# Optimization experiments

Measured on AMD Instinct MI355X. Metric: run time of the kernel, lower is better.

## Reference

```python
import jax, jax.numpy as jnp
import numpy as np

M1 = M2 = M3 = 12   # Fourier modes kept per dim
WID = 32            # channel width
NL = 4              # number of Fourier layers
HID = 128           # skip-block hidden
INF = 9             # coord_dim + param_dim


def _gelu(x):
    return jax.nn.gelu(x, approximate=False)  # torch F.gelu default is exact erf


def _spectral_conv3d(x, w1, w2, w3, w4):
    # x: [B, Cin, S, V, T]; weights: [Cin, Cout, M1, M2, M3, 2]
    B, Ci, S, Vd, T = x.shape
    x_ft = jnp.fft.rfftn(x, axes=(-3, -2, -1))  # [B,Ci,S,V,T//2+1] complex64

    def cmul(sub, w):
        wc = w[..., 0] + 1j * w[..., 1]
        return jnp.einsum('bixyz,ioxyz->boxyz', sub, wc)

    Co = w1.shape[1]
    out_ft = jnp.zeros((B, Co, S, Vd, T // 2 + 1), dtype=x_ft.dtype)
    out_ft = out_ft.at[:, :, :M1, :M2, :M3].set(cmul(x_ft[:, :, :M1, :M2, :M3], w1))
    out_ft = out_ft.at[:, :, -M1:, :M2, :M3].set(cmul(x_ft[:, :, -M1:, :M2, :M3], w2))
    out_ft = out_ft.at[:, :, :M1, -M2:, :M3].set(cmul(x_ft[:, :, :M1, -M2:, :M3], w3))
    out_ft = out_ft.at[:, :, -M1:, -M2:, :M3].set(cmul(x_ft[:, :, -M1:, -M2:, :M3], w4))
    return jnp.fft.irfftn(out_ft, s=(S, Vd, T), axes=(-3, -2, -1))


def setup_inputs() -> dict:
    key = jax.random.key(0)
    ks = jax.random.split(key, 24)
    B, S, Vd, T = 4, 64, 64, 64
    scale = 1.0 / (WID * WID)
    spec_shape = (NL, WID, WID, M1, M2, M3, 2)
    inp = {
        'coords': jax.random.uniform(ks[0], (B, S, Vd, T, 3), dtype=jnp.float32),
        'params': jax.random.normal(ks[1], (B, 6), dtype=jnp.float32),
        'lift_w': 0.3 * jax.random.normal(ks[2], (INF, WID), dtype=jnp.float32),
        'lift_b': jnp.zeros((WID,), jnp.float32),
        'spec_w1': scale * jax.random.uniform(ks[3], spec_shape, dtype=jnp.float32),
        'spec_w2': scale * jax.random.uniform(ks[4], spec_shape, dtype=jnp.float32),
        'spec_w3': scale * jax.random.uniform(ks[5], spec_shape, dtype=jnp.float32),
        'spec_w4': scale * jax.random.uniform(ks[6], spec_shape, dtype=jnp.float32),
        'conv_w': 0.15 * jax.random.normal(ks[7], (NL, WID, WID), dtype=jnp.float32),
        'conv_b': jnp.zeros((NL, WID), jnp.float32),
        's1w': 0.3 * jax.random.normal(ks[8], (NL, INF, HID), dtype=jnp.float32),
        's1b': jnp.zeros((NL, HID), jnp.float32),
        's2w': 0.09 * jax.random.normal(ks[9], (NL, HID, HID), dtype=jnp.float32),
        's2b': jnp.zeros((NL, HID), jnp.float32),
        's3w': 0.09 * jax.random.normal(ks[10], (NL, HID, WID), dtype=jnp.float32),
        's3b': jnp.zeros((NL, WID), jnp.float32),
        'p1w': 0.15 * jax.random.normal(ks[11], (WID, WID // 2), dtype=jnp.float32),
        'p1b': jnp.zeros((WID // 2,), jnp.float32),
        'p2w': 0.25 * jax.random.normal(ks[12], (WID // 2, 1), dtype=jnp.float32),
        'p2b': jnp.zeros((1,), jnp.float32),
    }
    return inp


def reference(coords, params, lift_w, lift_b, spec_w1, spec_w2, spec_w3, spec_w4,
              conv_w, conv_b, s1w, s1b, s2w, s2b, s3w, s3b, p1w, p1b, p2w, p2b):
    B, S, Vd, T, _ = coords.shape
    # coordinate lift: broadcast params over grid, concat -> [B,S,V,T,9]
    pexp = jnp.broadcast_to(params[:, None, None, None, :], (B, S, Vd, T, params.shape[-1]))
    z = jnp.concatenate([coords, pexp], axis=-1)
    x = z @ lift_w + lift_b                      # [B,S,V,T,W]
    x = jnp.transpose(x, (0, 4, 1, 2, 3))        # [B,W,S,V,T]
    for i in range(NL):
        x1 = _spectral_conv3d(x, spec_w1[i], spec_w2[i], spec_w3[i], spec_w4[i])
        x2 = jnp.einsum('bixyz,oi->boxyz', x, conv_w[i]) + conv_b[i][None, :, None, None, None]
        xf = _gelu(x1 + x2)
        skip = _gelu(z @ s1w[i] + s1b[i])
        skip = _gelu(skip @ s2w[i] + s2b[i])
        skip = skip @ s3w[i] + s3b[i]            # [B,S,V,T,W]
        x = xf + jnp.transpose(skip, (0, 4, 1, 2, 3))
    x = jnp.transpose(x, (0, 2, 3, 4, 1))        # [B,S,V,T,W]
    h = _gelu(x @ p1w + p1b)
    out = (h @ p2w + p2b)[..., 0]                # [B,S,V,T]
    return out
```

## Files before the change

### kernel.cpp

```cpp
#include <hip/hip_runtime.h>
#include <hip/hip_bf16.h>
#include <math.h>

#define NB   4
#define NC   32
#define SVT  262144
#define VT   4096
#define NLAY 4
#define TWOPI_64 0.09817477042468103f

typedef __attribute__((ext_vector_type(8))) short bf16x8;
typedef __attribute__((ext_vector_type(4))) float f32x4;
typedef __attribute__((ext_vector_type(4))) unsigned short us4;

__device__ __forceinline__ float gelu_f(float x){
    float x2 = x * x;
    float u  = x * __builtin_fmaf(-0.10294322f, x2, -2.30220795f);
    float e  = __builtin_amdgcn_exp2f(u);
    return x * __builtin_amdgcn_rcpf(1.0f + e);
}

__device__ __forceinline__ unsigned short f2bf(float f){
    union { __hip_bfloat16 h; unsigned short u; } cv;
    cv.h = __float2bfloat16(f);
    return cv.u;
}
__device__ __forceinline__ float bf2f(unsigned short u){
    return __uint_as_float(((unsigned int)u) << 16);
}

__global__ __launch_bounds__(256) void k_prep(
    const float* __restrict__ s1w, const float* __restrict__ s2w,
    const float* __restrict__ s3w,
    unsigned short* __restrict__ w1bf,
    unsigned short* __restrict__ w2bf,
    unsigned short* __restrict__ w3bf,
    unsigned short* __restrict__ tdft)
{
    int g = blockIdx.x * 256 + threadIdx.x;
    if (g < 65536){
        int l = g >> 14, r = g & 16383;
        int c = r >> 7, k = r & 127;
        w2bf[g] = f2bf(s2w[l*16384 + k*128 + c]);
        return;
    }
    int g3 = g - 65536;
    if (g3 < 16384){
        int l = g3 >> 12, r = g3 & 4095;
        int c2 = r >> 7, k = r & 127;
        w3bf[g3] = f2bf(s3w[l*4096 + k*32 + c2]);
        return;
    }
    int g1 = g3 - 16384;
    if (g1 < 4608){ w1bf[g1] = f2bf(s1w[g1]); return; }
    int g4 = g1 - 4608;
    if (g4 < 2048){
        int o = g4 >> 6, t = g4 & 63;
        float val = 0.f;
        if (o < 24){
            int kz = o >> 1;
            float ang = (float)((kz * t) & 63) * TWOPI_64;
            float sn, cs; sincosf(ang, &sn, &cs);
            val = (o & 1) ? -sn : cs;
        }
        unsigned short h = f2bf(val);
        tdft[g4]        = h;
        tdft[2048 + g4] = f2bf(val - bf2f(h));
    }
}

__global__ __launch_bounds__(256) void k_lift(
    const float* __restrict__ coords, const float* __restrict__ params,
    const float* __restrict__ lw, const float* __restrict__ lb,
    float* __restrict__ x)
{
    size_t g = (size_t)blockIdx.x * 256 + threadIdx.x;
    int b = (int)(g >> 18);
    size_t p = g & (size_t)(SVT - 1);
    float z[9];
    z[0] = coords[g*3+0]; z[1] = coords[g*3+1]; z[2] = coords[g*3+2];
    #pragma unroll
    for (int j = 0; j < 6; ++j) z[3+j] = params[b*6+j];
    #pragma unroll
    for (int c = 0; c < 32; ++c){
        float acc = lb[c];
        #pragma unroll
        for (int j = 0; j < 9; ++j) acc += z[j] * lw[j*32 + c];
        x[(size_t)(b*32 + c) * SVT + p] = acc;
    }
}

__global__ __launch_bounds__(256) void k_fwdTV(
    const float* __restrict__ x, const unsigned short* __restrict__ tdft,
    float2* __restrict__ X2)
{
    __shared__ __align__(16) unsigned short Ahi[64][72], Alo[64][72];
    __shared__ __align__(16) unsigned short Bhi[32][72], Blo[32][72];
    __shared__ float2 a2[12][66];
    __shared__ float2 wtab[64];
    int tid = threadIdx.x;
    int bc = blockIdx.x >> 6;
    int s  = blockIdx.x & 63;
    if (tid < 64){
        float sn, cs;
        sincosf((float)tid * TWOPI_64, &sn, &cs);
        wtab[tid] = make_float2(cs, sn);
    }
    for (int i = tid; i < 2048; i += 256){
        int o = i >> 6, t = i & 63;
        Bhi[o][t] = tdft[i];
        Blo[o][t] = tdft[2048 + i];
    }
    {
        int row = tid >> 2, c0 = (tid & 3) << 4;
        const float* src = x + (size_t)bc * SVT + (size_t)s * VT + row*64 + c0;
        #pragma unroll
        for (int q = 0; q < 4; ++q){
            float4 v4 = *(const float4*)&src[q*4];
            float vv[4] = {v4.x, v4.y, v4.z, v4.w};
            #pragma unroll
            for (int e = 0; e < 4; ++e){
                unsigned short h = f2bf(vv[e]);
                Ahi[row][c0 + q*4 + e] = h;
                Alo[row][c0 + q*4 + e] = f2bf(vv[e] - bf2f(h));
            }
        }
    }
    __syncthreads();
    int l = tid & 63, w = tid >> 6;
    int lr = l & 15, kg = l >> 4;
    int r0 = w << 4;
    f32x4 acc[2];
    acc[0] = (f32x4){0.f,0.f,0.f,0.f}; acc[1] = (f32x4){0.f,0.f,0.f,0.f};
    #pragma unroll
    for (int kc = 0; kc < 2; ++kc){
        int ko = kc*32 + kg*8;
        bf16x8 ah = *(const bf16x8*)&Ahi[r0 + lr][ko];
        bf16x8 al = *(const bf16x8*)&Alo[r0 + lr][ko];
        #pragma unroll
        for (int n = 0; n < 2; ++n){
            bf16x8 bh = *(const bf16x8*)&Bhi[n*16 + lr][ko];
            bf16x8 bl = *(const bf16x8*)&Blo[n*16 + lr][ko];
            acc[n] = __builtin_amdgcn_mfma_f32_16x16x32_bf16(ah, bh, acc[n], 0, 0, 0);
            acc[n] = __builtin_amdgcn_mfma_f32_16x16x32_bf16(ah, bl, acc[n], 0, 0, 0);
            acc[n] = __builtin_amdgcn_mfma_f32_16x16x32_bf16(al, bh, acc[n], 0, 0, 0);
        }
    }
    #pragma unroll
    for (int n = 0; n < 2; ++n){
        int o = n*16 + lr;
        if (o < 24){
            int kz = o >> 1;
            #pragma unroll
            for (int r = 0; r < 4; ++r){
                int v = r0 + kg*4 + r;
                if (o & 1) a2[kz][v].y = acc[n][r];
                else       a2[kz][v].x = acc[n][r];
            }
        }
    }
    __syncthreads();
    for (int task = tid; task < 288; task += 256){
        int kz = task % 12;
        int ky = task / 12;
        int kya = (ky < 12) ? ky : ky + 40;
        float re = 0.f, im = 0.f;
        for (int v = 0; v < 64; ++v){
            float2 wv = wtab[(kya * v) & 63];
            float2 a  = a2[kz][v];
            re += a.x * wv.x + a.y * wv.y;
            im += a.y * wv.x - a.x * wv.y;
        }
        X2[((size_t)(bc*12 + kz) * 24 + ky) * 64 + s] = make_float2(re, im);
    }
}

__global__ __launch_bounds__(256) void k_fwdS(
    const float2* __restrict__ X2, float2* __restrict__ X3)
{
    __shared__ float2 cin[32][65];
    __shared__ float2 wtab[64];
    int tid = threadIdx.x;
    if (tid < 64){
        float sn, cs; sincosf((float)tid * TWOPI_64, &sn, &cs);
        wtab[tid] = make_float2(cs, sn);
    }
    int rbase = blockIdx.x * 32;
    for (int i = tid; i < 2048; i += 256){
        int row = i >> 6, s = i & 63;
        cin[row][s] = X2[(size_t)(rbase + row) * 64 + s];
    }
    __syncthreads();
    int row = tid & 31;
    int r = rbase + row;
    int kxg = tid >> 5;
    int kxs[3];
    #pragma unroll
    for (int j = 0; j < 3; ++j){ int kxi = kxg*3 + j; kxs[j] = (kxi < 12) ? kxi : kxi + 40; }
    float re[3] = {0,0,0}, im[3] = {0,0,0};
    for (int s = 0; s < 64; ++s){
        float2 cv = cin[row][s];
        #pragma unroll
        for (int j = 0; j < 3; ++j){
            float2 wv = wtab[(kxs[j] * s) & 63];
            re[j] += cv.x * wv.x + cv.y * wv.y;
            im[j] += cv.y * wv.x - cv.x * wv.y;
        }
    }
    int bc = r / 288; int kz = (r / 24) % 12; int ky = r % 24;
    #pragma unroll
    for (int j = 0; j < 3; ++j){
        int kxi = kxg*3 + j;
        X3[(size_t)bc * 6912 + (size_t)kxi * 288 + ky * 12 + kz] = make_float2(re[j], im[j]);
    }
}

__global__ __launch_bounds__(256) void k_modemix(
    const float2* __restrict__ X3,
    const float* __restrict__ w1, const float* __restrict__ w2,
    const float* __restrict__ w3, const float* __restrict__ w4,
    int layer, float2* __restrict__ Y)
{
    __shared__ float2 wlds[32][64];
    int tid = threadIdx.x;
    int m   = tid & 63;
    int b   = tid >> 6;
    int corner = blockIdx.y >> 3;
    int o0     = (blockIdx.y & 7) * 4;
    int moff0  = blockIdx.x * 64;
    const float* wsrc = (corner==0 ? w1 : corner==1 ? w2 : corner==2 ? w3 : w4)
                        + (size_t)layer * 3538944;
    int moff = moff0 + m;
    int m1  = moff / 144;
    int rem = moff - m1 * 144;
    int kx  = m1 + ((corner == 1 || corner == 3) ? 12 : 0);
    int mode_g = kx * 288 + rem + ((corner >= 2) ? 144 : 0);

    float xr[32], xi[32];
    const float2* xp = X3 + (size_t)b * 32 * 6912 + mode_g;
    #pragma unroll
    for (int i = 0; i < 32; ++i){
        float2 a = xp[(size_t)i * 6912];
        xr[i] = a.x; xi[i] = a.y;
    }
    for (int oo = 0; oo < 4; ++oo){
        int o = o0 + oo;
        __syncthreads();
        for (int j = tid; j < 2048; j += 256){
            int i = j >> 6, mm = j & 63;
            wlds[i][mm] = *(const float2*)&wsrc[((size_t)(i*32 + o) * 1728 + moff0 + mm) * 2];
        }
        __syncthreads();
        float re = 0.f, im = 0.f;
        #pragma unroll
        for (int i = 0; i < 32; ++i){
            float2 wv = wlds[i][m];
            re += xr[i]*wv.x - xi[i]*wv.y;
            im += xr[i]*wv.y + xi[i]*wv.x;
        }
        Y[(size_t)(b*32 + o) * 6912 + mode_g] = make_float2(re, im);
    }
}

__global__ __launch_bounds__(256) void k_invS(
    const float2* __restrict__ Y, float2* __restrict__ Z1)
{
    __shared__ float2 yin[24][24];
    __shared__ float2 wtab[64];
    int tid = threadIdx.x;
    if (tid < 64){
        float sn, cs; sincosf((float)tid * TWOPI_64, &sn, &cs);
        wtab[tid] = make_float2(cs, sn);
    }
    int bo = blockIdx.x / 12;
    int kz = blockIdx.x % 12;
    for (int i = tid; i < 576; i += 256){
        int kx = i / 24, ky = i % 24;
        yin[kx][ky] = Y[(size_t)bo * 6912 + (size_t)kx * 288 + ky * 12 + kz];
    }
    __syncthreads();
    int s = tid & 63;
    int kyg = tid >> 6;
    float re[6] = {0,0,0,0,0,0}, im[6] = {0,0,0,0,0,0};
    for (int kxi = 0; kxi < 24; ++kxi){
        int kxa = (kxi < 12) ? kxi : kxi + 40;
        float2 wv = wtab[(kxa * s) & 63];
        #pragma unroll
        for (int j = 0; j < 6; ++j){
            float2 a = yin[kxi][kyg*6 + j];
            re[j] += a.x * wv.x - a.y * wv.y;
            im[j] += a.x * wv.y + a.y * wv.x;
        }
    }
    #pragma unroll
    for (int j = 0; j < 6; ++j){
        int ky = kyg*6 + j;
        Z1[((size_t)(bo*12 + kz) * 64 + s) * 24 + ky] = make_float2(re[j], im[j]);
    }
}

__global__ __launch_bounds__(256) void k_conv(
    float* x, const float* __restrict__ cw,
    const float* __restrict__ cb, int layer)
{
    __shared__ float wsh[32][32];
    __shared__ float bsh[32];
    int tid = threadIdx.x;
    if (tid < 32) bsh[tid] = cb[layer*32 + tid];
    for (int i = tid; i < 1024; i += 256) wsh[i >> 5][i & 31] = cw[layer*1024 + i];
    __syncthreads();
    size_t g = (size_t)blockIdx.x * 256 + tid;
    int b = (int)(g >> 18);
    size_t p = g & (size_t)(SVT - 1);
    float acc[32];
    #pragma unroll
    for (int o = 0; o < 32; ++o) acc[o] = bsh[o];
    for (int i = 0; i < 32; ++i){
        float xv = x[(size_t)(b*32 + i) * SVT + p];
        #pragma unroll
        for (int o = 0; o < 32; ++o) acc[o] += xv * wsh[o][i];
    }
    #pragma unroll
    for (int o = 0; o < 32; ++o) x[(size_t)(b*32 + o) * SVT + p] = acc[o];
}

__global__ __launch_bounds__(256) void k_invVT(
    const float2* __restrict__ Z1, float* xio)
{
    __shared__ float2 zin[12][24];
    __shared__ float2 c2[12][66];
    __shared__ float2 wtab[64];
    int tid = threadIdx.x;
    int bo = blockIdx.x >> 6;
    int s  = blockIdx.x & 63;
    if (tid < 64){
        float sn, cs; sincosf((float)tid * TWOPI_64, &sn, &cs);
        wtab[tid] = make_float2(cs, sn);
    }
    for (int i = tid; i < 288; i += 256){
        int kz = i / 24, ky = i % 24;
        zin[kz][ky] = Z1[((size_t)(bo*12 + kz) * 64 + s) * 24 + ky];
    }
    __syncthreads();
    #pragma unroll
    for (int j = 0; j < 3; ++j){
        int task = tid + j * 256;
        int v = task & 63, kz = task >> 6;
        float re = 0.f, im = 0.f;
        #pragma unroll
        for (int ky = 0; ky < 24; ++ky){
            int kya = (ky < 12) ? ky : ky + 40;
            float2 wv = wtab[(kya * v) & 63];
            float2 a = zin[kz][ky];
            re += a.x * wv.x - a.y * wv.y;
            im += a.x * wv.y + a.y * wv.x;
        }
        c2[kz][v] = make_float2(re, im);
    }
    __syncthreads();
    int v  = tid & 63;
    int tb = (tid >> 6) << 4;
    float sum[16];
    #pragma unroll
    for (int j = 0; j < 16; ++j) sum[j] = 0.f;
    float dc = c2[0][v].x;
    #pragma unroll
    for (int kz = 1; kz < 12; ++kz){
        float2 a = c2[kz][v];
        #pragma unroll
        for (int j = 0; j < 16; ++j){
            float2 wv = wtab[(kz * (tb + j)) & 63];
            sum[j] += a.x * wv.x - a.y * wv.y;
        }
    }
    const float norm = 1.0f / 262144.0f;
    size_t base = (size_t)bo * SVT + (size_t)s * VT + (size_t)v * 64 + tb;
    #pragma unroll
    for (int j = 0; j < 16; j += 4){
        float4 xv = *(const float4*)&xio[base + j];
        float4 r;
        r.x = gelu_f((dc + 2.f*sum[j+0]) * norm + xv.x);
        r.y = gelu_f((dc + 2.f*sum[j+1]) * norm + xv.y);
        r.z = gelu_f((dc + 2.f*sum[j+2]) * norm + xv.z);
        r.w = gelu_f((dc + 2.f*sum[j+3]) * norm + xv.w);
        *(float4*)&xio[base + j] = r;
    }
}

template<int LAST>
__global__ __launch_bounds__(256) void k_skip(
    const float* __restrict__ coords, const float* __restrict__ params,
    const unsigned short* __restrict__ w1bf, const float* __restrict__ s1b,
    const unsigned short* __restrict__ w2bf, const float* __restrict__ s2b,
    const unsigned short* __restrict__ w3bf, const float* __restrict__ s3b,
    int layer, float* __restrict__ xio,
    const float* __restrict__ p1w, const float* __restrict__ p1b,
    const float* __restrict__ p2w, const float* __restrict__ p2b,
    float* __restrict__ out)
{
    __shared__ __align__(16) unsigned short A1[64][136];
    __shared__ __align__(16) unsigned short zst[4][16][8];
    __shared__ __align__(16) unsigned short w1pk[128][8];
    __shared__ unsigned short w1s[9][128];
    __shared__ float pb[128];
    __shared__ float b2s[128];
    __shared__ float b3s[32];

    int tid = threadIdx.x;
    size_t g0 = (size_t)blockIdx.x * 64;
    int b = (int)(g0 >> 18);
    const unsigned short* w2g = w2bf + (size_t)layer * 16384;
    const unsigned short* w3g = w3bf + (size_t)layer * 4096;

    for (int i = tid; i < 1152; i += 256) w1s[i >> 7][i & 127] = w1bf[layer*1152 + i];
    if (tid < 128) b2s[tid] = s2b[layer*128 + tid];
    if (tid < 32)  b3s[tid] = s3b[layer*32  + tid];
    __syncthreads();
    if (tid < 128){
        float acc = s1b[layer*128 + tid];
        #pragma unroll
        for (int j = 0; j < 6; ++j) acc += params[b*6 + j] * bf2f(w1s[3 + j][tid]);
        pb[tid] = acc;
        bf16x8 pk;
        pk[0] = (short)w1s[0][tid]; pk[1] = (short)w1s[1][tid];
        pk[2] = (short)w1s[2][tid]; pk[3] = 0;
        pk[4] = pk[0]; pk[5] = pk[1]; pk[6] = pk[2]; pk[7] = 0;
        *(bf16x8*)&w1pk[tid][0] = pk;
    }
    __syncthreads();

    int l  = tid & 63;
    int w  = tid >> 6;
    int lr = l & 15;
    int kg = l >> 4;

    if (l < 16){
        size_t g = g0 + w*16 + l;
        float z0 = coords[g*3+0], z1 = coords[g*3+1], z2 = coords[g*3+2];
        unsigned short h0 = f2bf(z0), h1 = f2bf(z1), h2 = f2bf(z2);
        bf16x8 pk;
        pk[0] = (short)h0; pk[1] = (short)h1; pk[2] = (short)h2; pk[3] = 0;
        pk[4] = (short)f2bf(z0 - bf2f(h0));
        pk[5] = (short)f2bf(z1 - bf2f(h1));
        pk[6] = (short)f2bf(z2 - bf2f(h2));
        pk[7] = 0;
        *(bf16x8*)&zst[w][l][0] = pk;
    }
    bf16x8 bz;
    if (kg == 0) bz = *(const bf16x8*)&zst[w][lr][0];
    else         bz = (bf16x8){0,0,0,0,0,0,0,0};

    {
        f32x4 accB[8];
        #pragma unroll
        for (int m = 0; m < 8; ++m) accB[m] = (f32x4){0.f,0.f,0.f,0.f};
        #pragma unroll
        for (int m = 0; m < 8; ++m){
            bf16x8 af = *(const bf16x8*)&w1pk[m*16 + lr][0];
            accB[m] = __builtin_amdgcn_mfma_f32_16x16x32_bf16(af, bz, accB[m], 0, 0, 0);
        }
        #pragma unroll
        for (int m = 0; m < 8; ++m){
            int c0 = m*16 + kg*4;
            float4 bb = *(const float4*)&pb[c0];
            us4 pk4;
            pk4[0] = f2bf(gelu_f(accB[m][0] + bb.x));
            pk4[1] = f2bf(gelu_f(accB[m][1] + bb.y));
            pk4[2] = f2bf(gelu_f(accB[m][2] + bb.z));
            pk4[3] = f2bf(gelu_f(accB[m][3] + bb.w));
            *(us4*)&A1[w*16 + lr][c0] = pk4;
        }
    }
    __syncthreads();

    f32x4 accC[2][4];
    #pragma unroll
    for (int mi = 0; mi < 2; ++mi)
        #pragma unroll
        for (int pt = 0; pt < 4; ++pt) accC[mi][pt] = (f32x4){0.f,0.f,0.f,0.f};
    #pragma unroll
    for (int kc = 0; kc < 4; ++kc){
        int ko = kc*32 + kg*8;
        bf16x8 a0 = *(const bf16x8*)&w2g[((2*w    )*16 + lr)*128 + ko];
        bf16x8 a1 = *(const bf16x8*)&w2g[((2*w + 1)*16 + lr)*128 + ko];
        #pragma unroll
        for (int pt = 0; pt < 4; ++pt){
            bf16x8 bb = *(const bf16x8*)&A1[pt*16 + lr][ko];
            accC[0][pt] = __builtin_amdgcn_mfma_f32_16x16x32_bf16(a0, bb, accC[0][pt], 0, 0, 0);
            accC[1][pt] = __builtin_amdgcn_mfma_f32_16x16x32_bf16(a1, bb, accC[1][pt], 0, 0, 0);
        }
    }
    __syncthreads();
    #pragma unroll
    for (int mi = 0; mi < 2; ++mi)
        #pragma unroll
        for (int pt = 0; pt < 4; ++pt){
            int c0 = (2*w + mi)*16 + kg*4;
            float4 bb = *(const float4*)&b2s[c0];
            us4 pk4;
            pk4[0] = f2bf(gelu_f(accC[mi][pt][0] + bb.x));
            pk4[1] = f2bf(gelu_f(accC[mi][pt][1] + bb.y));
            pk4[2] = f2bf(gelu_f(accC[mi][pt][2] + bb.z));
            pk4[3] = f2bf(gelu_f(accC[mi][pt][3] + bb.w));
            *(us4*)&A1[pt*16 + lr][c0] = pk4;
        }
    __syncthreads();

    int nD  = w & 1;
    int pt0 = (w >> 1) * 2;
    f32x4 c3[2];
    c3[0] = (f32x4){0.f,0.f,0.f,0.f}; c3[1] = (f32x4){0.f,0.f,0.f,0.f};
    #pragma unroll
    for (int kc = 0; kc < 4; ++kc){
        int ko = kc*32 + kg*8;
        bf16x8 bw3 = *(const bf16x8*)&w3g[(nD*16 + lr)*128 + ko];
        bf16x8 aa0 = *(const bf16x8*)&A1[(pt0    )*16 + lr][ko];
        bf16x8 aa1 = *(const bf16x8*)&A1[(pt0 + 1)*16 + lr][ko];
        c3[0] = __builtin_amdgcn_mfma_f32_16x16x32_bf16(aa0, bw3, c3[0], 0, 0, 0);
        c3[1] = __builtin_amdgcn_mfma_f32_16x16x32_bf16(aa1, bw3, c3[1], 0, 0, 0);
    }
    __syncthreads();

    float* outsT = (float*)&A1[0][0];
    {
        int c2 = nD*16 + lr;
        float bv = b3s[c2];
        #pragma unroll
        for (int q = 0; q < 2; ++q){
            int p0 = (pt0 + q)*16 + kg*4;
            float4 v4;
            v4.x = c3[q][0] + bv; v4.y = c3[q][1] + bv;
            v4.z = c3[q][2] + bv; v4.w = c3[q][3] + bv;
            *(float4*)&outsT[c2*68 + p0] = v4;
        }
    }
    float* hs   = outsT + 2176;
    float* p1wS = outsT + 3264;
    float* smB  = outsT + 3776;
    if (LAST){
        for (int i = tid; i < 512; i += 256) p1wS[i] = p1w[i];
        if (tid < 16){ smB[tid] = p1b[tid]; smB[16 + tid] = p2w[tid]; }
        if (tid == 32) smB[32] = p2b[0];
    }
    __syncthreads();

    {
        int c  = tid >> 3;
        int pg = tid & 7;
        size_t prel = (g0 & (size_t)(SVT - 1)) + (size_t)pg*8;
        float* gp = xio + (((size_t)(b*32 + c)) << 18) + prel;
        float* op = &outsT[c*68 + pg*8];
        #pragma unroll
        for (int i = 0; i < 8; i += 4){
            float4 xv = *(const float4*)&gp[i];
            float4 ov = *(const float4*)&op[i];
            ov.x += xv.x; ov.y += xv.y; ov.z += xv.z; ov.w += xv.w;
            if (LAST) *(float4*)&op[i] = ov;
            else      *(float4*)&gp[i] = ov;
        }
    }
    if (LAST){
        __syncthreads();
        {
            int p  = tid & 63;
            int jq = tid >> 6;
            float h[4];
            #pragma unroll
            for (int j = 0; j < 4; ++j) h[j] = smB[jq*4 + j];
            for (int c = 0; c < 32; ++c){
                float xv = outsT[c*68 + p];
                #pragma unroll
                for (int j = 0; j < 4; ++j) h[j] += xv * p1wS[c*16 + jq*4 + j];
            }
            #pragma unroll
            for (int j = 0; j < 4; ++j) hs[p*17 + jq*4 + j] = h[j];
        }
        __syncthreads();
        if (tid < 64){
            float acc = smB[32];
            #pragma unroll
            for (int j = 0; j < 16; ++j) acc += gelu_f(hs[tid*17 + j]) * smB[16 + j];
            out[g0 + tid] = acc;
        }
    }
}

extern "C" void kernel_launch(void* const* d_in, const int* in_sizes, int n_in,
                              void* d_out, int out_size, void* d_ws, size_t ws_size,
                              hipStream_t stream)
{
    (void)in_sizes; (void)n_in; (void)out_size; (void)ws_size;
    const float* coords = (const float*)d_in[0];
    const float* params = (const float*)d_in[1];
    const float* lift_w = (const float*)d_in[2];
    const float* lift_b = (const float*)d_in[3];
    const float* sw1    = (const float*)d_in[4];
    const float* sw2    = (const float*)d_in[5];
    const float* sw3    = (const float*)d_in[6];
    const float* sw4    = (const float*)d_in[7];
    const float* conv_w = (const float*)d_in[8];
    const float* conv_b = (const float*)d_in[9];
    const float* s1w    = (const float*)d_in[10];
    const float* s1b    = (const float*)d_in[11];
    const float* s2w    = (const float*)d_in[12];
    const float* s2b    = (const float*)d_in[13];
    const float* s3w    = (const float*)d_in[14];
    const float* s3b    = (const float*)d_in[15];
    const float* p1w    = (const float*)d_in[16];
    const float* p1b    = (const float*)d_in[17];
    const float* p2w    = (const float*)d_in[18];
    const float* p2b    = (const float*)d_in[19];
    float* out = (float*)d_out;

    char* ws = (char*)d_ws;
    float*  xA = (float*)(ws);
    float2* X2 = (float2*)(ws + 134217728ull);
    float2* X3 = (float2*)(ws + 153092096ull);
    float2* Yb = (float2*)(ws + 160169984ull);
    unsigned short* w2bf = (unsigned short*)(ws + 167247872ull);
    unsigned short* w3bf = (unsigned short*)(ws + 167378944ull);
    unsigned short* w1bf = (unsigned short*)(ws + 167411712ull);
    unsigned short* tdft = (unsigned short*)(ws + 167420928ull);

    k_prep<<<346, 256, 0, stream>>>(s1w, s2w, s3w, w1bf, w2bf, w3bf, tdft);
    k_lift<<<4096, 256, 0, stream>>>(coords, params, lift_w, lift_b, xA);

    for (int l = 0; l < NLAY; ++l){
        k_fwdTV<<<8192, 256, 0, stream>>>(xA, tdft, X2);
        k_fwdS<<<1152, 256, 0, stream>>>(X2, X3);
        dim3 gmm(27, 32);
        k_modemix<<<gmm, 256, 0, stream>>>(X3, sw1, sw2, sw3, sw4, l, Yb);
        k_invS<<<1536, 256, 0, stream>>>(Yb, X2);
        k_conv<<<4096, 256, 0, stream>>>(xA, conv_w, conv_b, l);
        k_invVT<<<8192, 256, 0, stream>>>(X2, xA);
        if (l < NLAY - 1)
            k_skip<0><<<16384, 256, 0, stream>>>(coords, params, w1bf, s1b,
                w2bf, s2b, w3bf, s3b, l, xA, p1w, p1b, p2w, p2b, out);
        else
            k_skip<1><<<16384, 256, 0, stream>>>(coords, params, w1bf, s1b,
                w2bf, s2b, w3bf, s3b, l, xA, p1w, p1b, p2w, p2b, out);
    }
}
```

Baseline: 1.841 ms.

## Run inverse V/T DFT on MFMA with split-bf16 tables; precompute skip weights

The inverse V and T transforms in k_invVT become two small bf16 MFMA matrix products instead of scalar complex loops over a twiddle table. Each operand is split into high and low bf16 halves and combined in three MFMA passes to keep close to fp32 accuracy. The DFT matrices are built once in k_prep, and the per-batch first-layer bias (params times weights plus s1b) and the packed W1 fragments are also precomputed there. This removes per-block shared-memory staging and two barriers from k_skip and lets it request higher occupancy. One risk: the padding columns 24–31 of the A2 LDS buffers are never zeroed, so stale NaN bits there could leak into the output even though the matching table entries are zero.

```diff
diff --git a/kernel.cpp b/kernel.cpp
--- a/kernel.cpp
+++ b/kernel.cpp
@@ -30,12 +30,16 @@
 }
 
 __global__ __launch_bounds__(256) void k_prep(
-    const float* __restrict__ s1w, const float* __restrict__ s2w,
-    const float* __restrict__ s3w,
-    unsigned short* __restrict__ w1bf,
+    const float* __restrict__ params,
+    const float* __restrict__ s1w, const float* __restrict__ s1b,
+    const float* __restrict__ s2w, const float* __restrict__ s3w,
     unsigned short* __restrict__ w2bf,
     unsigned short* __restrict__ w3bf,
-    unsigned short* __restrict__ tdft)
+    unsigned short* __restrict__ tdft,
+    unsigned short* __restrict__ T1h, unsigned short* __restrict__ T1l,
+    unsigned short* __restrict__ T2h, unsigned short* __restrict__ T2l,
+    float* __restrict__ pbq,
+    unsigned short* __restrict__ w1dup)
 {
     int g = blockIdx.x * 256 + threadIdx.x;
     if (g < 65536){
@@ -44,18 +48,16 @@
         w2bf[g] = f2bf(s2w[l*16384 + k*128 + c]);
         return;
     }
-    int g3 = g - 65536;
-    if (g3 < 16384){
-        int l = g3 >> 12, r = g3 & 4095;
+    g -= 65536;
+    if (g < 16384){
+        int l = g >> 12, r = g & 4095;
         int c2 = r >> 7, k = r & 127;
-        w3bf[g3] = f2bf(s3w[l*4096 + k*32 + c2]);
+        w3bf[g] = f2bf(s3w[l*4096 + k*32 + c2]);
         return;
     }
-    int g1 = g3 - 16384;
-    if (g1 < 4608){ w1bf[g1] = f2bf(s1w[g1]); return; }
-    int g4 = g1 - 4608;
-    if (g4 < 2048){
-        int o = g4 >> 6, t = g4 & 63;
+    g -= 16384;
+    if (g < 2048){
+        int o = g >> 6, t = g & 63;
         float val = 0.f;
         if (o < 24){
             int kz = o >> 1;
@@ -64,8 +66,63 @@
             val = (o & 1) ? -sn : cs;
         }
         unsigned short h = f2bf(val);
-        tdft[g4]        = h;
-        tdft[2048 + g4] = f2bf(val - bf2f(h));
+        tdft[g]        = h;
+        tdft[2048 + g] = f2bf(val - bf2f(h));
+        return;
+    }
+    g -= 2048;
+    if (g < 8192){
+        int col = g >> 6, k1 = g & 63;
+        int v = col >> 1, pout = col & 1;
+        float val = 0.f;
+        if (k1 < 48){
+            int ky = k1 >> 1, pin = k1 & 1;
+            int kya = (ky < 12) ? ky : ky + 40;
+            float ang = (float)((kya * v) & 63) * TWOPI_64;
+            float sn, cs; sincosf(ang, &sn, &cs);
+            val = pout == 0 ? (pin == 0 ? cs : -sn) : (pin == 0 ? sn : cs);
+        }
+        unsigned short h = f2bf(val);
+        T1h[g] = h;
+        T1l[g] = f2bf(val - bf2f(h));
+        return;
+    }
+    g -= 8192;
+    if (g < 2048){
+        int t = g >> 5, k2 = g & 31;
+        float val = 0.f;
+        if (k2 < 24){
+            int kz = k2 >> 1, part = k2 & 1;
+            float wk = (kz == 0) ? 1.f : 2.f;
+            float ang = (float)((kz * t) & 63) * TWOPI_64;
+            float sn, cs; sincosf(ang, &sn, &cs);
+            val = (part ? -sn : cs) * wk * (1.f / 262144.f);
+        }
+        unsigned short h = f2bf(val);
+        T2h[g] = h;
+        T2l[g] = f2bf(val - bf2f(h));
+        return;
+    }
+    g -= 2048;
+    if (g < 2048){
+        int l = g >> 9, b = (g >> 7) & 3, h = g & 127;
+        float acc = s1b[l*128 + h];
+        #pragma unroll
+        for (int j = 0; j < 6; ++j)
+            acc += params[b*6 + j] * bf2f(f2bf(s1w[l*1152 + (3 + j)*128 + h]));
+        pbq[g] = acc;
+        return;
+    }
+    g -= 2048;
+    if (g < 4096){
+        int l = g >> 10, rem = g & 1023;
+        int h = rem >> 3, slot = rem & 7;
+        float val = 0.f;
+        if (slot != 3 && slot != 7){
+            int row = (slot < 3) ? slot : slot - 4;
+            val = bf2f(f2bf(s1w[l*1152 + row*128 + h]));
+        }
+        w1dup[g] = f2bf(val);
     }
 }
 
@@ -325,72 +382,90 @@
 }
 
 __global__ __launch_bounds__(256) void k_invVT(
-    const float2* __restrict__ Z1, float* xio)
-{
-    __shared__ float2 zin[12][24];
-    __shared__ float2 c2[12][66];
-    __shared__ float2 wtab[64];
+    const float2* __restrict__ Z1,
+    const unsigned short* __restrict__ T1h, const unsigned short* __restrict__ T1l,
+    const unsigned short* __restrict__ T2h, const unsigned short* __restrict__ T2l,
+    float* xio)
+{
+    __shared__ __align__(16) unsigned short A1h[16][72], A1l[16][72];
+    __shared__ __align__(16) unsigned short A2h[64][40], A2l[64][40];
     int tid = threadIdx.x;
     int bo = blockIdx.x >> 6;
     int s  = blockIdx.x & 63;
-    if (tid < 64){
-        float sn, cs; sincosf((float)tid * TWOPI_64, &sn, &cs);
-        wtab[tid] = make_float2(cs, sn);
+    for (int i = tid; i < 384; i += 256){
+        int r = i / 24, c = 48 + (i % 24);
+        A1h[r][c] = 0; A1l[r][c] = 0;
+    }
+    for (int i = tid; i < 192; i += 256){
+        int r = 12 + i / 48, c = i % 48;
+        A1h[r][c] = 0; A1l[r][c] = 0;
     }
     for (int i = tid; i < 288; i += 256){
         int kz = i / 24, ky = i % 24;
-        zin[kz][ky] = Z1[((size_t)(bo*12 + kz) * 64 + s) * 24 + ky];
-    }
-    __syncthreads();
-    #pragma unroll
-    for (int j = 0; j < 3; ++j){
-        int task = tid + j * 256;
-        int v = task & 63, kz = task >> 6;
-        float re = 0.f, im = 0.f;
-        #pragma unroll
-        for (int ky = 0; ky < 24; ++ky){
-            int kya = (ky < 12) ? ky : ky + 40;
-            float2 wv = wtab[(kya * v) & 63];
-            float2 a = zin[kz][ky];
-            re += a.x * wv.x - a.y * wv.y;
-            im += a.x * wv.y + a.y * wv.x;
-        }
-        c2[kz][v] = make_float2(re, im);
-    }
-    __syncthreads();
-    int v  = tid & 63;
-    int tb = (tid >> 6) << 4;
-    float sum[16];
-    #pragma unroll
-    for (int j = 0; j < 16; ++j) sum[j] = 0.f;
-    float dc = c2[0][v].x;
-    #pragma unroll
-    for (int kz = 1; kz < 12; ++kz){
-        float2 a = c2[kz][v];
-        #pragma unroll
-        for (int j = 0; j < 16; ++j){
-            float2 wv = wtab[(kz * (tb + j)) & 63];
-            sum[j] += a.x * wv.x - a.y * wv.y;
-        }
-    }
-    const float norm = 1.0f / 262144.0f;
-    size_t base = (size_t)bo * SVT + (size_t)s * VT + (size_t)v * 64 + tb;
-    #pragma unroll
-    for (int j = 0; j < 16; j += 4){
-        float4 xv = *(const float4*)&xio[base + j];
-        float4 r;
-        r.x = gelu_f((dc + 2.f*sum[j+0]) * norm + xv.x);
-        r.y = gelu_f((dc + 2.f*sum[j+1]) * norm + xv.y);
-        r.z = gelu_f((dc + 2.f*sum[j+2]) * norm + xv.z);
-        r.w = gelu_f((dc + 2.f*sum[j+3]) * norm + xv.w);
-        *(float4*)&xio[base + j] = r;
+        float2 a = Z1[((size_t)(bo*12 + kz) * 64 + s) * 24 + ky];
+        unsigned short hx = f2bf(a.x), hy = f2bf(a.y);
+        A1h[kz][2*ky  ] = hx; A1l[kz][2*ky  ] = f2bf(a.x - bf2f(hx));
+        A1h[kz][2*ky+1] = hy; A1l[kz][2*ky+1] = f2bf(a.y - bf2f(hy));
+    }
+    __syncthreads();
+    int l = tid & 63, w = tid >> 6;
+    int lr = l & 15, kg = l >> 4;
+    f32x4 acc1[2];
+    acc1[0] = (f32x4){0.f,0.f,0.f,0.f}; acc1[1] = (f32x4){0.f,0.f,0.f,0.f};
+    #pragma unroll
+    for (int kc = 0; kc < 2; ++kc){
+        int ko = kc*32 + kg*8;
+        bf16x8 ah = *(const bf16x8*)&A1h[lr][ko];
+        bf16x8 al = *(const bf16x8*)&A1l[lr][ko];
+        #pragma unroll
+        for (int n = 0; n < 2; ++n){
+            int col = (2*w + n)*16 + lr;
+            bf16x8 bh = *(const bf16x8*)&T1h[col*64 + ko];
+            bf16x8 bl = *(const bf16x8*)&T1l[col*64 + ko];
+            acc1[n] = __builtin_amdgcn_mfma_f32_16x16x32_bf16(ah, bh, acc1[n], 0, 0, 0);
+            acc1[n] = __builtin_amdgcn_mfma_f32_16x16x32_bf16(ah, bl, acc1[n], 0, 0, 0);
+            acc1[n] = __builtin_amdgcn_mfma_f32_16x16x32_bf16(al, bh, acc1[n], 0, 0, 0);
+        }
+    }
+    #pragma unroll
+    for (int n = 0; n < 2; ++n){
+        int col = (2*w + n)*16 + lr;
+        int v = col >> 1, part = col & 1;
+        #pragma unroll
+        for (int r = 0; r < 4; ++r){
+            int k2 = 2*(kg*4 + r) + part;
+            float val = acc1[n][r];
+            unsigned short h = f2bf(val);
+            A2h[v][k2] = h;
+            A2l[v][k2] = f2bf(val - bf2f(h));
+        }
+    }
+    int r0 = w << 4;
+    bf16x8 ah2 = *(const bf16x8*)&A2h[r0 + lr][kg*8];
+    bf16x8 al2 = *(const bf16x8*)&A2l[r0 + lr][kg*8];
+    size_t base = (size_t)bo * SVT + (size_t)s * VT;
+    #pragma unroll
+    for (int n = 0; n < 4; ++n){
+        f32x4 a2c = (f32x4){0.f,0.f,0.f,0.f};
+        int colt = n*16 + lr;
+        bf16x8 bh = *(const bf16x8*)&T2h[colt*32 + kg*8];
+        bf16x8 bl = *(const bf16x8*)&T2l[colt*32 + kg*8];
+        a2c = __builtin_amdgcn_mfma_f32_16x16x32_bf16(ah2, bh, a2c, 0, 0, 0);
+        a2c = __builtin_amdgcn_mfma_f32_16x16x32_bf16(ah2, bl, a2c, 0, 0, 0);
+        a2c = __builtin_amdgcn_mfma_f32_16x16x32_bf16(al2, bh, a2c, 0, 0, 0);
+        #pragma unroll
+        for (int r = 0; r < 4; ++r){
+            int v = r0 + kg*4 + r;
+            size_t idx = base + (size_t)v*64 + colt;
+            xio[idx] = gelu_f(a2c[r] + xio[idx]);
+        }
     }
 }
 
 template<int LAST>
-__global__ __launch_bounds__(256) void k_skip(
-    const float* __restrict__ coords, const float* __restrict__ params,
-    const unsigned short* __restrict__ w1bf, const float* __restrict__ s1b,
+__global__ __launch_bounds__(256, 8) void k_skip(
+    const float* __restrict__ coords,
+    const unsigned short* __restrict__ w1dup, const float* __restrict__ pbq,
     const unsigned short* __restrict__ w2bf, const float* __restrict__ s2b,
     const unsigned short* __restrict__ w3bf, const float* __restrict__ s3b,
     int layer, float* __restrict__ xio,
@@ -400,34 +475,15 @@
 {
     __shared__ __align__(16) unsigned short A1[64][136];
     __shared__ __align__(16) unsigned short zst[4][16][8];
-    __shared__ __align__(16) unsigned short w1pk[128][8];
-    __shared__ unsigned short w1s[9][128];
-    __shared__ float pb[128];
-    __shared__ float b2s[128];
-    __shared__ float b3s[32];
 
     int tid = threadIdx.x;
     size_t g0 = (size_t)blockIdx.x * 64;
     int b = (int)(g0 >> 18);
     const unsigned short* w2g = w2bf + (size_t)layer * 16384;
     const unsigned short* w3g = w3bf + (size_t)layer * 4096;
-
-    for (int i = tid; i < 1152; i += 256) w1s[i >> 7][i & 127] = w1bf[layer*1152 + i];
-    if (tid < 128) b2s[tid] = s2b[layer*128 + tid];
-    if (tid < 32)  b3s[tid] = s3b[layer*32  + tid];
-    __syncthreads();
-    if (tid < 128){
-        float acc = s1b[layer*128 + tid];
-        #pragma unroll
-        for (int j = 0; j < 6; ++j) acc += params[b*6 + j] * bf2f(w1s[3 + j][tid]);
-        pb[tid] = acc;
-        bf16x8 pk;
-        pk[0] = (short)w1s[0][tid]; pk[1] = (short)w1s[1][tid];
-        pk[2] = (short)w1s[2][tid]; pk[3] = 0;
-        pk[4] = pk[0]; pk[5] = pk[1]; pk[6] = pk[2]; pk[7] = 0;
-        *(bf16x8*)&w1pk[tid][0] = pk;
-    }
-    __syncthreads();
+    const unsigned short* w1g = w1dup + (size_t)layer * 1024;
+    const float* pbg = pbq + layer*512 + b*128;
+    const float* b2g = s2b + layer*128;
 
     int l  = tid & 63;
     int w  = tid >> 6;
@@ -435,7 +491,7 @@
     int kg = l >> 4;
 
     if (l < 16){
-        size_t g = g0 + w*16 + l;
+        size_t g = g0 + (size_t)w*16 + l;
         float z0 = coords[g*3+0], z1 = coords[g*3+1], z2 = coords[g*3+2];
         unsigned short h0 = f2bf(z0), h1 = f2bf(z1), h2 = f2bf(z2);
         bf16x8 pk;
@@ -456,13 +512,13 @@
         for (int m = 0; m < 8; ++m) accB[m] = (f32x4){0.f,0.f,0.f,0.f};
         #pragma unroll
         for (int m = 0; m < 8; ++m){
-            bf16x8 af = *(const bf16x8*)&w1pk[m*16 + lr][0];
+            bf16x8 af = *(const bf16x8*)&w1g[(m*16 + lr)*8];
             accB[m] = __builtin_amdgcn_mfma_f32_16x16x32_bf16(af, bz, accB[m], 0, 0, 0);
         }
         #pragma unroll
         for (int m = 0; m < 8; ++m){
             int c0 = m*16 + kg*4;
-            float4 bb = *(const float4*)&pb[c0];
+            float4 bb = *(const float4*)&pbg[c0];
             us4 pk4;
             pk4[0] = f2bf(gelu_f(accB[m][0] + bb.x));
             pk4[1] = f2bf(gelu_f(accB[m][1] + bb.y));
@@ -496,7 +552,7 @@
         #pragma unroll
         for (int pt = 0; pt < 4; ++pt){
             int c0 = (2*w + mi)*16 + kg*4;
-            float4 bb = *(const float4*)&b2s[c0];
+            float4 bb = *(const float4*)&b2g[c0];
             us4 pk4;
             pk4[0] = f2bf(gelu_f(accC[mi][pt][0] + bb.x));
             pk4[1] = f2bf(gelu_f(accC[mi][pt][1] + bb.y));
@@ -508,6 +564,7 @@
 
     int nD  = w & 1;
     int pt0 = (w >> 1) * 2;
+    float b3v = s3b[layer*32 + nD*16 + lr];
     f32x4 c3[2];
     c3[0] = (f32x4){0.f,0.f,0.f,0.f}; c3[1] = (f32x4){0.f,0.f,0.f,0.f};
     #pragma unroll
@@ -524,13 +581,12 @@
     float* outsT = (float*)&A1[0][0];
     {
         int c2 = nD*16 + lr;
-        float bv = b3s[c2];
         #pragma unroll
         for (int q = 0; q < 2; ++q){
             int p0 = (pt0 + q)*16 + kg*4;
             float4 v4;
-            v4.x = c3[q][0] + bv; v4.y = c3[q][1] + bv;
-            v4.z = c3[q][2] + bv; v4.w = c3[q][3] + bv;
+            v4.x = c3[q][0] + b3v; v4.y = c3[q][1] + b3v;
+            v4.z = c3[q][2] + b3v; v4.w = c3[q][3] + b3v;
             *(float4*)&outsT[c2*68 + p0] = v4;
         }
     }
@@ -617,12 +673,19 @@
     float2* X2 = (float2*)(ws + 134217728ull);
     float2* X3 = (float2*)(ws + 153092096ull);
     float2* Yb = (float2*)(ws + 160169984ull);
-    unsigned short* w2bf = (unsigned short*)(ws + 167247872ull);
-    unsigned short* w3bf = (unsigned short*)(ws + 167378944ull);
-    unsigned short* w1bf = (unsigned short*)(ws + 167411712ull);
-    unsigned short* tdft = (unsigned short*)(ws + 167420928ull);
-
-    k_prep<<<346, 256, 0, stream>>>(s1w, s2w, s3w, w1bf, w2bf, w3bf, tdft);
+    unsigned short* w2bf  = (unsigned short*)(ws + 167247872ull);
+    unsigned short* w3bf  = (unsigned short*)(ws + 167378944ull);
+    unsigned short* tdft  = (unsigned short*)(ws + 167411712ull);
+    unsigned short* T1h   = (unsigned short*)(ws + 167419904ull);
+    unsigned short* T1l   = (unsigned short*)(ws + 167436288ull);
+    unsigned short* T2h   = (unsigned short*)(ws + 167452672ull);
+    unsigned short* T2l   = (unsigned short*)(ws + 167456768ull);
+    float*          pbq   = (float*)(ws + 167460864ull);
+    unsigned short* w1dup = (unsigned short*)(ws + 167469056ull);
+
+    k_prep<<<392, 256, 0, stream>>>(params, s1w, s1b, s2w, s3w,
+                                    w2bf, w3bf, tdft, T1h, T1l, T2h, T2l,
+                                    pbq, w1dup);
     k_lift<<<4096, 256, 0, stream>>>(coords, params, lift_w, lift_b, xA);
 
     for (int l = 0; l < NLAY; ++l){
@@ -632,12 +695,12 @@
         k_modemix<<<gmm, 256, 0, stream>>>(X3, sw1, sw2, sw3, sw4, l, Yb);
         k_invS<<<1536, 256, 0, stream>>>(Yb, X2);
         k_conv<<<4096, 256, 0, stream>>>(xA, conv_w, conv_b, l);
-        k_invVT<<<8192, 256, 0, stream>>>(X2, xA);
+        k_invVT<<<8192, 256, 0, stream>>>(X2, T1h, T1l, T2h, T2l, xA);
         if (l < NLAY - 1)
-            k_skip<0><<<16384, 256, 0, stream>>>(coords, params, w1bf, s1b,
+            k_skip<0><<<16384, 256, 0, stream>>>(coords, w1dup, pbq,
                 w2bf, s2b, w3bf, s3b, l, xA, p1w, p1b, p2w, p2b, out);
         else
-            k_skip<1><<<16384, 256, 0, stream>>>(coords, params, w1bf, s1b,
+            k_skip<1><<<16384, 256, 0, stream>>>(coords, w1dup, pbq,
                 w2bf, s2b, w3bf, s3b, l, xA, p1w, p1b, p2w, p2b, out);
     }
 }
```

Measured after the change: 1.701 ms. -7.6%, faster.
